# Kernel optimization log

Hardware: AMD Instinct MI355X
Metric: run time of the kernel (lower is better)

## Reference

```python
import jax, jax.numpy as jnp
import numpy as np

B, T, F, D, NL, V = 16, 1024, 80, 512, 3, 28


def _ln(x, g, b, eps=1e-5):
    m = jnp.mean(x, axis=-1, keepdims=True)
    v = jnp.mean((x - m) ** 2, axis=-1, keepdims=True)
    return (x - m) * jax.lax.rsqrt(v + eps) * g + b


def _sru_layer(x, W, wc, bias, g, beta):
    # x: [T, B, din]; W: [din, k*d] (k=4 when din != d, else k=3)
    d = wc.shape[0] // 2
    xn = _ln(x, g, beta)                       # layer_norm=True: LN on layer input
    U = jnp.einsum('tbi,ij->tbj', xn, W)       # [T, B, k*d]
    u0, u1, u2 = U[..., :d], U[..., d:2 * d], U[..., 2 * d:3 * d]
    xres = U[..., 3 * d:4 * d] if W.shape[1] == 4 * d else x  # highway input
    vf, vr = wc[:d], wc[d:]
    bf, br = bias[:d], bias[d:]

    def step(c, inp):
        a0, a1, a2, xr = inp
        f = jax.nn.sigmoid(a1 + vf * c + bf)
        r = jax.nn.sigmoid(a2 + vr * c + br)
        c2 = f * c + (1.0 - f) * a0
        h = r * c2 + (1.0 - r) * xr
        return c2, h

    c0 = jnp.zeros((x.shape[1], d), x.dtype)
    _, h = jax.lax.scan(step, c0, (u0, u1, u2, xres))
    return h


def _lstm_layer(x, wih, whh, bih, bhh):
    # x: [T, B, d]; torch gate order i, f, g, o
    d = whh.shape[1]
    gx = jnp.einsum('tbi,gi->tbg', x, wih) + bih + bhh  # precompute input gates

    def step(carry, gxt):
        h, c = carry
        gts = gxt + h @ whh.T
        i, f, gg, o = jnp.split(gts, 4, axis=-1)
        c2 = jax.nn.sigmoid(f) * c + jax.nn.sigmoid(i) * jnp.tanh(gg)
        h2 = jax.nn.sigmoid(o) * jnp.tanh(c2)
        return (h2, c2), h2

    nb = x.shape[1]
    init = (jnp.zeros((nb, d), x.dtype), jnp.zeros((nb, d), x.dtype))
    _, h = jax.lax.scan(step, init, gx)
    return h


def _forward(x, sru_w0, sru_wc0, sru_b0, sru_ln0_g, sru_ln0_b,
             sru_w, sru_wc, sru_b, sru_ln_g, sru_ln_b,
             lstm_ln_g, lstm_ln_b, lstm_wih, lstm_whh, lstm_bih, lstm_bhh,
             cls_ln_g, cls_ln_b, cls_w):
    h = jnp.transpose(x, (1, 0, 2))  # [T, B, F]
    h = _sru_layer(h, sru_w0, sru_wc0, sru_b0, sru_ln0_g, sru_ln0_b)
    for i in range(sru_w.shape[0]):  # 7 remaining SRU layers (8 total)
        h = _sru_layer(h, sru_w[i], sru_wc[i], sru_b[i], sru_ln_g[i], sru_ln_b[i])
    for i in range(lstm_wih.shape[0]):  # LSTM blocks: LN -> LSTM (dropout off, eval)
        hn = _ln(h, lstm_ln_g[i], lstm_ln_b[i])
        h = _lstm_layer(hn, lstm_wih[i], lstm_whh[i], lstm_bih[i], lstm_bhh[i])
    h = jnp.transpose(h, (1, 0, 2))  # [B, T, D]
    h = _ln(h, cls_ln_g, cls_ln_b)
    return h @ cls_w                 # [B, T, V+1]


def setup_inputs() -> dict:
    key = jax.random.key(0)
    ks = jax.random.split(key, 8)
    n = lambda k, s, sc: jax.random.normal(k, s, jnp.float32) * sc
    sF, sD = 1.0 / np.sqrt(F), 1.0 / np.sqrt(D)
    return {
        'x': n(ks[0], (B, T, F), 1.0),
        'sru_w0': n(ks[1], (F, 4 * D), sF),
        'sru_wc0': n(ks[2], (2 * D,), 0.1),
        'sru_b0': jnp.zeros((2 * D,), jnp.float32),
        'sru_ln0_g': jnp.ones((F,), jnp.float32),
        'sru_ln0_b': jnp.zeros((F,), jnp.float32),
        'sru_w': n(ks[3], (7, D, 3 * D), sD),
        'sru_wc': n(ks[4], (7, 2 * D), 0.1),
        'sru_b': jnp.zeros((7, 2 * D), jnp.float32),
        'sru_ln_g': jnp.ones((7, D), jnp.float32),
        'sru_ln_b': jnp.zeros((7, D), jnp.float32),
        'lstm_ln_g': jnp.ones((NL, D), jnp.float32),
        'lstm_ln_b': jnp.zeros((NL, D), jnp.float32),
        'lstm_wih': n(ks[5], (NL, 4 * D, D), sD),
        'lstm_whh': n(ks[6], (NL, 4 * D, D), sD),
        'lstm_bih': jnp.zeros((NL, 4 * D), jnp.float32),
        'lstm_bhh': jnp.zeros((NL, 4 * D), jnp.float32),
        'cls_ln_g': jnp.ones((D,), jnp.float32),
        'cls_ln_b': jnp.zeros((D,), jnp.float32),
        'cls_w': n(ks[7], (D, V + 1), sD),
    }


def reference(x, sru_w0, sru_wc0, sru_b0, sru_ln0_g, sru_ln0_b,
              sru_w, sru_wc, sru_b, sru_ln_g, sru_ln_b,
              lstm_ln_g, lstm_ln_b, lstm_wih, lstm_whh, lstm_bih, lstm_bhh,
              cls_ln_g, cls_ln_b, cls_w):
    return _forward(x, sru_w0, sru_wc0, sru_b0, sru_ln0_g, sru_ln0_b,
                    sru_w, sru_wc, sru_b, sru_ln_g, sru_ln_b,
                    lstm_ln_g, lstm_ln_b, lstm_wih, lstm_whh, lstm_bih, lstm_bhh,
                    cls_ln_g, cls_ln_b, cls_w)
```

## Files before the change

kernel.cpp:

```cpp
#include <hip/hip_runtime.h>
#include <stdint.h>
#include <stddef.h>

#define B_ 16
#define T_ 1024
#define F_ 80
#define D_ 512
#define M_ 16384
#define VO 29
#define SENT 0x7FC07FC0u

typedef float f32x4 __attribute__((ext_vector_type(4)));
typedef short s16x8 __attribute__((ext_vector_type(8)));
typedef unsigned short u16x8 __attribute__((ext_vector_type(8)));

static __device__ __forceinline__ unsigned short f2bf(float f) {
    union { float f; unsigned u; } v; v.f = f;
    unsigned r = v.u + 0x7FFFu + ((v.u >> 16) & 1u);
    return (unsigned short)(r >> 16);
}
static __device__ __forceinline__ float bf2f(unsigned short h) {
    union { unsigned u; float f; } v; v.u = ((unsigned)h) << 16; return v.f;
}
static __device__ __forceinline__ void split2(float v, unsigned short& hi, unsigned short& lo) {
    hi = f2bf(v);
    lo = f2bf(v - bf2f(hi));
}
static __device__ __forceinline__ float sigm(float x) {
    return 1.0f / (1.0f + __expf(-x));
}
static __device__ __forceinline__ float fast_tanh(float x) {
    return 1.0f - 2.0f / (__expf(2.0f * x) + 1.0f);
}
static __device__ __forceinline__ float wred(float v) {
    #pragma unroll
    for (int off = 1; off < 64; off <<= 1) v += __shfl_xor(v, off, 64);
    return v;
}
static __device__ __forceinline__ float ldf_agent(const float* p) {
    unsigned u = __hip_atomic_load((const unsigned*)p, __ATOMIC_RELAXED, __HIP_MEMORY_SCOPE_AGENT);
    union { unsigned u; float f; } c; c.u = u; return c.f;
}
static __device__ __forceinline__ void stf_agent(float* p, float v) {
    union { float f; unsigned u; } c; c.f = v;
    __hip_atomic_store((unsigned*)p, c.u, __ATOMIC_RELAXED, __HIP_MEMORY_SCOPE_AGENT);
}
static __device__ __forceinline__ void gload16(const void* g, void* lds) {
    __builtin_amdgcn_global_load_lds(
        (const __attribute__((address_space(1))) void*)g,
        (__attribute__((address_space(3))) void*)lds, 16, 0, 0);
}

__global__ __launch_bounds__(256) void conv_w0(const float* __restrict__ W,
        unsigned short* __restrict__ Bh, unsigned short* __restrict__ Bl) {
    int gid = blockIdx.x * 256 + threadIdx.x;
    int n = gid / 96, k = gid - n * 96;
    float v = (k < 80) ? W[(size_t)k * 2048 + n] : 0.0f;
    unsigned short h, l; split2(v, h, l);
    Bh[gid] = h; Bl[gid] = l;
}
__global__ __launch_bounds__(256) void conv_sruw1(const float* __restrict__ W,
        unsigned short* __restrict__ Bh, unsigned short* __restrict__ Bl) {
    int gid = blockIdx.x * 256 + threadIdx.x;
    int n = gid >> 9, k = gid & 511;
    float v = W[(size_t)k * 1536 + n];
    unsigned short h, lo; split2(v, h, lo);
    Bh[gid] = h; Bl[gid] = lo;
}
__global__ __launch_bounds__(256) void conv_split(const float* __restrict__ W,
        unsigned short* __restrict__ Oh, unsigned short* __restrict__ Ol, int n) {
    int gid = blockIdx.x * 256 + threadIdx.x;
    if (gid < n) {
        unsigned short h, l; split2(W[gid], h, l);
        Oh[gid] = h; Ol[gid] = l;
    }
}
__global__ __launch_bounds__(256) void sent_fill(unsigned int* __restrict__ buf, int n) {
    int gid = blockIdx.x * 256 + threadIdx.x;
    if (gid < n)
        __hip_atomic_store(&buf[gid], SENT, __ATOMIC_RELAXED, __HIP_MEMORY_SCOPE_AGENT);
}
__global__ void zero_ctl(unsigned int* c) {
    if (threadIdx.x < 160)
        __hip_atomic_store(&c[threadIdx.x], 0u, __ATOMIC_RELAXED, __HIP_MEMORY_SCOPE_AGENT);
}

__global__ __launch_bounds__(256) void ln80_kernel(const float* __restrict__ x,
        const float* __restrict__ g, const float* __restrict__ bta,
        unsigned short* __restrict__ xh, unsigned short* __restrict__ xl) {
    int w = threadIdx.x >> 6, lane = threadIdx.x & 63;
    int row = blockIdx.x * 4 + w;
    int b = row & 15, t = row >> 4;
    const float* xr = x + ((size_t)b * T_ + t) * F_;
    float v0 = xr[lane];
    float v1 = (lane < 16) ? xr[64 + lane] : 0.0f;
    float mean = wred(v0 + v1) * (1.0f / 80.0f);
    float d0 = v0 - mean;
    float d1 = (lane < 16) ? (v1 - mean) : 0.0f;
    float var = wred(d0 * d0 + d1 * d1) * (1.0f / 80.0f);
    float rstd = rsqrtf(var + 1e-5f);
    float o0 = d0 * rstd * g[lane] + bta[lane];
    unsigned short h, l; split2(o0, h, l);
    xh[(size_t)row * 96 + lane] = h;
    xl[(size_t)row * 96 + lane] = l;
    if (lane < 32) {
        unsigned short hv = 0, lv = 0;
        if (lane < 16) {
            float o1 = d1 * rstd * g[64 + lane] + bta[64 + lane];
            split2(o1, hv, lv);
        }
        xh[(size_t)row * 96 + 64 + lane] = hv;
        xl[(size_t)row * 96 + 64 + lane] = lv;
    }
}

__global__ __launch_bounds__(256) void ln512_bf16(const float* __restrict__ hsrc,
        const float* __restrict__ g, const float* __restrict__ bta,
        unsigned short* __restrict__ oh, unsigned short* __restrict__ ol) {
    int w = threadIdx.x >> 6, lane = threadIdx.x & 63;
    size_t row = (size_t)blockIdx.x * 4 + w;
    const float* hr = hsrc + row * D_;
    float4 p0 = *(const float4*)(hr + lane * 8);
    float4 p1 = *(const float4*)(hr + lane * 8 + 4);
    float s = p0.x + p0.y + p0.z + p0.w + p1.x + p1.y + p1.z + p1.w;
    float mean = wred(s) * (1.0f / 512.0f);
    float d[8] = {p0.x - mean, p0.y - mean, p0.z - mean, p0.w - mean,
                  p1.x - mean, p1.y - mean, p1.z - mean, p1.w - mean};
    float q = 0.f;
    #pragma unroll
    for (int i = 0; i < 8; ++i) q += d[i] * d[i];
    float rstd = rsqrtf(wred(q) * (1.0f / 512.0f) + 1e-5f);
    const float* gp = g + lane * 8;
    const float* bp = bta + lane * 8;
    u16x8 vh, vl;
    #pragma unroll
    for (int i = 0; i < 8; ++i) {
        float o = d[i] * rstd * gp[i] + bp[i];
        unsigned short hh, ll; split2(o, hh, ll);
        vh[i] = hh; vl[i] = ll;
    }
    *(u16x8*)(oh + row * D_ + lane * 8) = vh;
    *(u16x8*)(ol + row * D_ + lane * 8) = vl;
}

__global__ __launch_bounds__(256) void ln512_f32(const float* __restrict__ hsrc,
        const float* __restrict__ g, const float* __restrict__ bta,
        float* __restrict__ o) {
    int w = threadIdx.x >> 6, lane = threadIdx.x & 63;
    size_t row = (size_t)blockIdx.x * 4 + w;
    const float* hr = hsrc + row * D_;
    float4 p0 = *(const float4*)(hr + lane * 8);
    float4 p1 = *(const float4*)(hr + lane * 8 + 4);
    float s = p0.x + p0.y + p0.z + p0.w + p1.x + p1.y + p1.z + p1.w;
    float mean = wred(s) * (1.0f / 512.0f);
    float d[8] = {p0.x - mean, p0.y - mean, p0.z - mean, p0.w - mean,
                  p1.x - mean, p1.y - mean, p1.z - mean, p1.w - mean};
    float q = 0.f;
    #pragma unroll
    for (int i = 0; i < 8; ++i) q += d[i] * d[i];
    float rstd = rsqrtf(wred(q) * (1.0f / 512.0f) + 1e-5f);
    const float* gp = g + lane * 8;
    const float* bp = bta + lane * 8;
    float* op = o + row * D_ + lane * 8;
    #pragma unroll
    for (int i = 0; i < 8; ++i) op[i] = d[i] * rstd * gp[i] + bp[i];
}

__global__ __launch_bounds__(256) void gemm_split(
        const unsigned short* __restrict__ Ah, const unsigned short* __restrict__ Al,
        const unsigned short* __restrict__ Bh, const unsigned short* __restrict__ Bl,
        float* __restrict__ C, int N, int Kp,
        const float* __restrict__ bias0, const float* __restrict__ bias1) {
    __shared__ __align__(16) unsigned short sAh[4096];
    __shared__ __align__(16) unsigned short sAl[4096];
    __shared__ __align__(16) unsigned short sBh[4096];
    __shared__ __align__(16) unsigned short sBl[4096];
    const int tid = threadIdx.x;
    const int wv = tid >> 6, lane = tid & 63;
    const int c_ = lane & 15, r_ = lane >> 4;
    const int wr = wv >> 1, wc = wv & 1;
    const int mBase = blockIdx.y * 128, nBase = blockIdx.x * 128;

    const int row0 = tid >> 2, row1 = 64 + row0;
    const int sp = tid & 3;
    const int x0 = (row0 & 3) ^ ((row0 >> 2) & 3);
    const int x1 = (row1 & 3) ^ ((row1 >> 2) & 3);
    const size_t gA0 = (size_t)(mBase + row0) * Kp + (size_t)((sp ^ x0) * 8);
    const size_t gA1 = (size_t)(mBase + row1) * Kp + (size_t)((sp ^ x1) * 8);
    const size_t gB0 = (size_t)(nBase + row0) * Kp + (size_t)((sp ^ x0) * 8);
    const size_t gB1 = (size_t)(nBase + row1) * Kp + (size_t)((sp ^ x1) * 8);
    const int ldsW = wv * 1024;

    int offA[4], offB[4];
    #pragma unroll
    for (int f = 0; f < 4; ++f) {
        int ra = wr * 64 + f * 16 + c_;
        int xa = (ra & 3) ^ ((ra >> 2) & 3);
        offA[f] = ra * 32 + ((r_ ^ xa) * 8);
        int rb = wc * 64 + f * 16 + c_;
        int xb = (rb & 3) ^ ((rb >> 2) & 3);
        offB[f] = rb * 32 + ((r_ ^ xb) * 8);
    }

    f32x4 acc[4][4] = {};
    for (int kt = 0; kt < Kp; kt += 32) {
        gload16(Ah + gA0 + kt, (char*)sAh + ldsW);
        gload16(Ah + gA1 + kt, (char*)sAh + 4096 + ldsW);
        gload16(Al + gA0 + kt, (char*)sAl + ldsW);
        gload16(Al + gA1 + kt, (char*)sAl + 4096 + ldsW);
        gload16(Bh + gB0 + kt, (char*)sBh + ldsW);
        gload16(Bh + gB1 + kt, (char*)sBh + 4096 + ldsW);
        gload16(Bl + gB0 + kt, (char*)sBl + ldsW);
        gload16(Bl + gB1 + kt, (char*)sBl + 4096 + ldsW);
        __syncthreads();
        s16x8 ah[4], al[4], bh[4], bl[4];
        #pragma unroll
        for (int f = 0; f < 4; ++f) {
            ah[f] = *(const s16x8*)&sAh[offA[f]];
            al[f] = *(const s16x8*)&sAl[offA[f]];
            bh[f] = *(const s16x8*)&sBh[offB[f]];
            bl[f] = *(const s16x8*)&sBl[offB[f]];
        }
        #pragma unroll
        for (int mf = 0; mf < 4; ++mf) {
            #pragma unroll
            for (int nf = 0; nf < 4; ++nf) {
                acc[mf][nf] = __builtin_amdgcn_mfma_f32_16x16x32_bf16(ah[mf], bh[nf], acc[mf][nf], 0, 0, 0);
                acc[mf][nf] = __builtin_amdgcn_mfma_f32_16x16x32_bf16(al[mf], bh[nf], acc[mf][nf], 0, 0, 0);
                acc[mf][nf] = __builtin_amdgcn_mfma_f32_16x16x32_bf16(ah[mf], bl[nf], acc[mf][nf], 0, 0, 0);
            }
        }
        __syncthreads();
    }
    #pragma unroll
    for (int mf = 0; mf < 4; ++mf) {
        #pragma unroll
        for (int r = 0; r < 4; ++r) {
            int m = mBase + wr * 64 + mf * 16 + r_ * 4 + r;
            float* crow = C + (size_t)m * N + nBase + wc * 64;
            #pragma unroll
            for (int nf = 0; nf < 4; ++nf) {
                int n = nBase + wc * 64 + nf * 16 + c_;
                float v = acc[mf][nf][r];
                if (bias0) v += bias0[n];
                if (bias1) v += bias1[n];
                crow[nf * 16 + c_] = v;
            }
        }
    }
}

__global__ __launch_bounds__(64) void sru_rec(const float* __restrict__ U, int NU,
        const float* __restrict__ xprev, const float* __restrict__ wc,
        const float* __restrict__ bias, float* __restrict__ hout) {
    int gid = blockIdx.x * 64 + threadIdx.x;
    int d = gid & (D_ - 1), b = gid >> 9;
    float vf = wc[d], vr = wc[D_ + d];
    float bf = bias[d], br = bias[D_ + d];
    const float* u0 = U + d;
    const float* u1 = U + D_ + d;
    const float* u2 = U + 2 * D_ + d;
    const float* xr;  size_t xstride;
    if (xprev) { xr = xprev + d; xstride = D_; }
    else       { xr = U + 3 * (size_t)D_ + d; xstride = (size_t)NU; }
    float* ho = hout + d;
    float c = 0.f;
    #pragma unroll 4
    for (int t = 0; t < T_; ++t) {
        size_t row = (size_t)(t * 16 + b);
        float a0 = u0[row * NU];
        float a1 = u1[row * NU];
        float a2 = u2[row * NU];
        float xv = xr[row * xstride];
        float f = sigm(a1 + vf * c + bf);
        float r = sigm(a2 + vr * c + br);
        c = f * c + (1.f - f) * a0;
        float h = r * c + (1.f - r) * xv;
        ho[row * D_] = h;
    }
}


template <int MODE>
static __device__ void lstm_role(int wg, const float* gxsrc,
        const unsigned short* Wh, const unsigned short* Wl,
        unsigned* ring, const unsigned* crewflags, unsigned* myLprog,
        const unsigned* consCprog, float* hout) {
    __shared__ __align__(16) unsigned short hH[16][520];
    __shared__ __align__(16) unsigned short hL[16][520];
    __shared__ float G[16][132];
    const int tid = threadIdx.x;
    const int w = tid >> 6, lane = tid & 63;
    const int c_ = lane & 15, r_ = lane >> 4;

    s16x8 bh0[16], bh1[16], bl0[16], bl1[16];
    {
        size_t R0 = (size_t)(w * 512 + wg * 32 + c_) * 512;
        size_t R1 = R0 + 16 * 512;
        #pragma unroll
        for (int ks = 0; ks < 16; ++ks) {
            bh0[ks] = *(const s16x8*)(Wh + R0 + ks * 32 + r_ * 8);
            bh1[ks] = *(const s16x8*)(Wh + R1 + ks * 32 + r_ * 8);
            bl0[ks] = *(const s16x8*)(Wl + R0 + ks * 32 + r_ * 8);
            bl1[ks] = *(const s16x8*)(Wl + R1 + ks * 32 + r_ * 8);
        }
    }
    for (int i = tid; i < 16 * 520; i += 256) {
        ((unsigned short*)hH)[i] = 0;
        ((unsigned short*)hL)[i] = 0;
    }
    const int eb = tid >> 4;
    const int ed = (tid * 2) & 31;
    float cc0 = 0.f, cc1 = 0.f;
    const int col0 = w * 512 + wg * 32 + c_;
    const int hidx = (eb * 512 + wg * 32 + ed) >> 1;

    float gxv0[4], gxv1[4];
    if (MODE == 0) {
        #pragma unroll
        for (int r = 0; r < 4; ++r) {
            int bt = r_ * 4 + r;
            gxv0[r] = gxsrc[(size_t)bt * 2048 + col0];
            gxv1[r] = gxsrc[(size_t)bt * 2048 + col0 + 16];
        }
    } else {
        while (true) {
            int f = (int)__hip_atomic_load(&crewflags[lane & 31],
                                           __ATOMIC_RELAXED, __HIP_MEMORY_SCOPE_AGENT);
            if (__all(f >= 1)) break;
            __builtin_amdgcn_s_sleep(1);
        }
        #pragma unroll
        for (int r = 0; r < 4; ++r) {
            int bt = r_ * 4 + r;
            gxv0[r] = ldf_agent(gxsrc + (size_t)bt * 2048 + col0);
            gxv1[r] = ldf_agent(gxsrc + (size_t)bt * 2048 + col0 + 16);
        }
    }
    int pcur = 0, pnxt = 8192, pthr = 16384;
    __syncthreads();

    for (int t = 0; t < T_; ++t) {
        if (MODE == 1 && tid == 0)
            __hip_atomic_store(&myLprog[wg], (unsigned)t, __ATOMIC_RELAXED, __HIP_MEMORY_SCOPE_AGENT);
        if (consCprog) {
            int lim = t - 1;
            while (true) {
                int p = (int)__hip_atomic_load(&consCprog[lane & 31],
                                               __ATOMIC_RELAXED, __HIP_MEMORY_SCOPE_AGENT);
                if (__all(p >= lim)) break;
                __builtin_amdgcn_s_sleep(2);
            }
        }
        __hip_atomic_store(&ring[pnxt + hidx], SENT, __ATOMIC_RELAXED, __HIP_MEMORY_SCOPE_AGENT);
        __hip_atomic_store(&ring[pnxt + 4096 + hidx], SENT, __ATOMIC_RELAXED, __HIP_MEMORY_SCOPE_AGENT);
        f32x4 acc0 = {0.f, 0.f, 0.f, 0.f};
        f32x4 acc1 = {0.f, 0.f, 0.f, 0.f};
        #pragma unroll
        for (int ks = 0; ks < 16; ++ks) {
            s16x8 ah = *(const s16x8*)&hH[c_][ks * 32 + r_ * 8];
            s16x8 al = *(const s16x8*)&hL[c_][ks * 32 + r_ * 8];
            acc0 = __builtin_amdgcn_mfma_f32_16x16x32_bf16(ah, bh0[ks], acc0, 0, 0, 0);
            acc1 = __builtin_amdgcn_mfma_f32_16x16x32_bf16(ah, bh1[ks], acc1, 0, 0, 0);
            acc0 = __builtin_amdgcn_mfma_f32_16x16x32_bf16(al, bh0[ks], acc0, 0, 0, 0);
            acc1 = __builtin_amdgcn_mfma_f32_16x16x32_bf16(al, bh1[ks], acc1, 0, 0, 0);
            acc0 = __builtin_amdgcn_mfma_f32_16x16x32_bf16(ah, bl0[ks], acc0, 0, 0, 0);
            acc1 = __builtin_amdgcn_mfma_f32_16x16x32_bf16(ah, bl1[ks], acc1, 0, 0, 0);
        }
        #pragma unroll
        for (int r = 0; r < 4; ++r) {
            int bt = r_ * 4 + r;
            G[bt][w * 32 + c_]      = acc0[r] + gxv0[r];
            G[bt][w * 32 + 16 + c_] = acc1[r] + gxv1[r];
        }
        __syncthreads();
        float iv0 = G[eb][ed],     fv0 = G[eb][32 + ed], gv0 = G[eb][64 + ed], ov0 = G[eb][96 + ed];
        float iv1 = G[eb][ed + 1], fv1 = G[eb][33 + ed], gv1 = G[eb][65 + ed], ov1 = G[eb][97 + ed];
        cc0 = sigm(fv0) * cc0 + sigm(iv0) * fast_tanh(gv0);
        cc1 = sigm(fv1) * cc1 + sigm(iv1) * fast_tanh(gv1);
        float h0 = sigm(ov0) * fast_tanh(cc0);
        float h1 = sigm(ov1) * fast_tanh(cc1);
        asm volatile("s_waitcnt vmcnt(0)" ::: "memory");
        unsigned short h0h, h0l, h1h, h1l;
        split2(h0, h0h, h0l); split2(h1, h1h, h1l);
        unsigned packH = (unsigned)h0h | ((unsigned)h1h << 16);
        unsigned packL = (unsigned)h0l | ((unsigned)h1l << 16);
        __hip_atomic_store(&ring[pcur + hidx], packH, __ATOMIC_RELAXED, __HIP_MEMORY_SCOPE_AGENT);
        __hip_atomic_store(&ring[pcur + 4096 + hidx], packL, __ATOMIC_RELAXED, __HIP_MEMORY_SCOPE_AGENT);
        if (hout) {
            size_t orow = (size_t)(t * 16 + eb) * D_ + wg * 32 + ed;
            hout[orow] = h0; hout[orow + 1] = h1;
        }
        if (t == T_ - 1) break;
        if (MODE == 0) {
            const float* gxr = gxsrc + (size_t)((t + 1) * 16) * 2048;
            #pragma unroll
            for (int r = 0; r < 4; ++r) {
                int bt = r_ * 4 + r;
                gxv0[r] = gxr[(size_t)bt * 2048 + col0];
                gxv1[r] = gxr[(size_t)bt * 2048 + col0 + 16];
            }
        } else {
            int need = t + 2;
            while (true) {
                int f = (int)__hip_atomic_load(&crewflags[lane & 31],
                                               __ATOMIC_RELAXED, __HIP_MEMORY_SCOPE_AGENT);
                if (__all(f >= need)) break;
                __builtin_amdgcn_s_sleep(1);
            }
            const float* gs = gxsrc + (size_t)((t + 1) & 3) * 32768;
            #pragma unroll
            for (int r = 0; r < 4; ++r) {
                int bt = r_ * 4 + r;
                gxv0[r] = ldf_agent(gs + (size_t)bt * 2048 + col0);
                gxv1[r] = ldf_agent(gs + (size_t)bt * 2048 + col0 + 16);
            }
        }
        unsigned long long vh[8], vl[8];
        unsigned badm = 0xFFFFu;
        while (true) {
            #pragma unroll
            for (int j = 0; j < 8; ++j) {
                int q = pcur + j * 512 + tid * 2;
                if (badm & (1u << j))
                    vh[j] = __hip_atomic_load((const unsigned long long*)&ring[q],
                                              __ATOMIC_RELAXED, __HIP_MEMORY_SCOPE_AGENT);
                if (badm & (1u << (8 + j)))
                    vl[j] = __hip_atomic_load((const unsigned long long*)&ring[q + 4096],
                                              __ATOMIC_RELAXED, __HIP_MEMORY_SCOPE_AGENT);
            }
            unsigned nb = 0u;
            #pragma unroll
            for (int j = 0; j < 8; ++j) {
                unsigned a0 = (unsigned)vh[j], a1 = (unsigned)(vh[j] >> 32);
                unsigned b0 = (unsigned)vl[j], b1 = (unsigned)(vl[j] >> 32);
                if (((a0 >> 16) == 0x7FC0u) || ((a1 >> 16) == 0x7FC0u)) nb |= 1u << j;
                if (((b0 >> 16) == 0x7FC0u) || ((b1 >> 16) == 0x7FC0u)) nb |= 1u << (8 + j);
            }
            badm = nb;
            if (!__any(badm != 0u)) break;
            __builtin_amdgcn_s_sleep(1);
        }
        #pragma unroll
        for (int j = 0; j < 8; ++j) {
            int q = j * 512 + tid * 2;
            int bb = q >> 8, dd = (q & 255) * 2;
            *(unsigned long long*)&hH[bb][dd] = vh[j];
            *(unsigned long long*)&hL[bb][dd] = vl[j];
        }
        __syncthreads();
        int tmp = pcur; pcur = pnxt; pnxt = pthr; pthr = tmp;
    }
}

static __device__ void crew_role(int cid, const unsigned* srcring, float* gxr,
        unsigned* flags, unsigned* cprog, const unsigned* lprog,
        const unsigned short* WihHp, const unsigned short* WihLp,
        const float* g, const float* bta,
        const float* bihp, const float* bhhp) {
    __shared__ __align__(16) unsigned short xnH[16][520];
    __shared__ __align__(16) unsigned short xnL[16][520];
    const int tid = threadIdx.x;
    const int w = tid >> 6, lane = tid & 63;
    const int c_ = lane & 15, r_ = lane >> 4;
    const int col = cid * 64 + w * 16 + c_;
    const int rr = w * 4 + r_;

    s16x8 bfh[16], bfl[16];
    {
        const unsigned short* wrH = WihHp + (size_t)col * 512;
        const unsigned short* wrL = WihLp + (size_t)col * 512;
        #pragma unroll
        for (int ks = 0; ks < 16; ++ks) {
            bfh[ks] = *(const s16x8*)(wrH + ks * 32 + r_ * 8);
            bfl[ks] = *(const s16x8*)(wrL + ks * 32 + r_ * 8);
        }
    }
    const float bias = bihp[col] + bhhp[col];
    float lg[32], lb[32];
    #pragma unroll
    for (int j = 0; j < 32; ++j) { lg[j] = g[c_ * 32 + j]; lb[j] = bta[c_ * 32 + j]; }

    for (int t = 0; t < T_; ++t) {
        const unsigned* sb = srcring + (t % 3) * 8192;
        const int qi = rr * 256 + c_ * 16;
        unsigned long long vh[8], vl[8];
        unsigned badm = 0xFFFFu;
        while (true) {
            #pragma unroll
            for (int j = 0; j < 8; ++j) {
                if (badm & (1u << j))
                    vh[j] = __hip_atomic_load((const unsigned long long*)&sb[qi + j * 2],
                                              __ATOMIC_RELAXED, __HIP_MEMORY_SCOPE_AGENT);
                if (badm & (1u << (8 + j)))
                    vl[j] = __hip_atomic_load((const unsigned long long*)&sb[4096 + qi + j * 2],
                                              __ATOMIC_RELAXED, __HIP_MEMORY_SCOPE_AGENT);
            }
            unsigned nb = 0u;
            #pragma unroll
            for (int j = 0; j < 8; ++j) {
                unsigned a0 = (unsigned)vh[j], a1 = (unsigned)(vh[j] >> 32);
                unsigned b0 = (unsigned)vl[j], b1 = (unsigned)(vl[j] >> 32);
                if (((a0 >> 16) == 0x7FC0u) || ((a1 >> 16) == 0x7FC0u)) nb |= 1u << j;
                if (((b0 >> 16) == 0x7FC0u) || ((b1 >> 16) == 0x7FC0u)) nb |= 1u << (8 + j);
            }
            badm = nb;
            if (!__any(badm != 0u)) break;
            __builtin_amdgcn_s_sleep(1);
        }
        float x[32];
        #pragma unroll
        for (int k = 0; k < 8; ++k) {
            unsigned ah = (unsigned)vh[k], bh = (unsigned)(vh[k] >> 32);
            unsigned al = (unsigned)vl[k], bl = (unsigned)(vl[k] >> 32);
            x[4 * k + 0] = bf2f((unsigned short)ah) + bf2f((unsigned short)al);
            x[4 * k + 1] = bf2f((unsigned short)(ah >> 16)) + bf2f((unsigned short)(al >> 16));
            x[4 * k + 2] = bf2f((unsigned short)bh) + bf2f((unsigned short)bl);
            x[4 * k + 3] = bf2f((unsigned short)(bh >> 16)) + bf2f((unsigned short)(bl >> 16));
        }
        float s = 0.f;
        #pragma unroll
        for (int j = 0; j < 32; ++j) s += x[j];
        #pragma unroll
        for (int m = 1; m < 16; m <<= 1) s += __shfl_xor(s, m, 64);
        float mean = s * (1.0f / 512.0f);
        float q = 0.f;
        #pragma unroll
        for (int j = 0; j < 32; ++j) { float d = x[j] - mean; q += d * d; }
        #pragma unroll
        for (int m = 1; m < 16; m <<= 1) q += __shfl_xor(q, m, 64);
        float rstd = rsqrtf(q * (1.0f / 512.0f) + 1e-5f);
        u16x8 ph[4], pl[4];
        #pragma unroll
        for (int j = 0; j < 32; ++j) {
            float o = (x[j] - mean) * rstd * lg[j] + lb[j];
            unsigned short hh, ll; split2(o, hh, ll);
            ph[j >> 3][j & 7] = (unsigned short)hh;
            pl[j >> 3][j & 7] = (unsigned short)ll;
        }
        #pragma unroll
        for (int jj = 0; jj < 4; ++jj) {
            *(u16x8*)&xnH[rr][c_ * 32 + jj * 8] = ph[jj];
            *(u16x8*)&xnL[rr][c_ * 32 + jj * 8] = pl[jj];
        }
        __syncthreads();
        if (tid == 0)
            __hip_atomic_store(&cprog[cid], (unsigned)(t + 1), __ATOMIC_RELAXED, __HIP_MEMORY_SCOPE_AGENT);
        f32x4 acc = {bias, bias, bias, bias};
        #pragma unroll
        for (int ks = 0; ks < 16; ++ks) {
            s16x8 axh = *(const s16x8*)&xnH[c_][ks * 32 + r_ * 8];
            s16x8 axl = *(const s16x8*)&xnL[c_][ks * 32 + r_ * 8];
            acc = __builtin_amdgcn_mfma_f32_16x16x32_bf16(axh, bfh[ks], acc, 0, 0, 0);
            acc = __builtin_amdgcn_mfma_f32_16x16x32_bf16(axl, bfh[ks], acc, 0, 0, 0);
            acc = __builtin_amdgcn_mfma_f32_16x16x32_bf16(axh, bfl[ks], acc, 0, 0, 0);
        }
        {
            int lim = t - 3;
            while (true) {
                int p = (int)__hip_atomic_load(&lprog[lane & 15],
                                               __ATOMIC_RELAXED, __HIP_MEMORY_SCOPE_AGENT);
                if (__all(p >= lim)) break;
                __builtin_amdgcn_s_sleep(2);
            }
        }
        float* gs = gxr + (size_t)(t & 3) * 32768;
        #pragma unroll
        for (int r = 0; r < 4; ++r)
            stf_agent(gs + (size_t)(r_ * 4 + r) * 2048 + col, acc[r]);
        asm volatile("s_waitcnt vmcnt(0)" ::: "memory");
        __syncthreads();
        if (tid == 0)
            __hip_atomic_store(&flags[cid], (unsigned)(t + 1), __ATOMIC_RELAXED, __HIP_MEMORY_SCOPE_AGENT);
    }
}

__global__ __launch_bounds__(256, 1) void lstm_pipe(
        const float* __restrict__ gx0,
        const unsigned short* __restrict__ WhhH, const unsigned short* __restrict__ WhhL,
        const unsigned short* __restrict__ WihH, const unsigned short* __restrict__ WihL,
        const float* __restrict__ lng, const float* __restrict__ lnb,
        const float* __restrict__ bih, const float* __restrict__ bhh,
        float* __restrict__ hout,
        unsigned* __restrict__ rings,
        float* __restrict__ gxr,
        unsigned* __restrict__ ctl) {
    const int bid = blockIdx.x;
    const size_t WSL = (size_t)2048 * 512;
    if (bid < 16) {
        lstm_role<0>(bid, gx0, WhhH, WhhL, rings,
                     nullptr, nullptr, ctl + 96, nullptr);
    } else if (bid < 32) {
        lstm_role<1>(bid - 16, gxr, WhhH + WSL, WhhL + WSL, rings + 24576,
                     ctl + 0, ctl + 64, ctl + 128, nullptr);
    } else if (bid < 48) {
        lstm_role<1>(bid - 32, gxr + 4 * 32768, WhhH + 2 * WSL, WhhL + 2 * WSL, rings + 2 * 24576,
                     ctl + 32, ctl + 80, nullptr, hout);
    } else if (bid < 80) {
        crew_role(bid - 48, rings, gxr, ctl + 0, ctl + 96, ctl + 64,
                  WihH, WihL, lng + 512, lnb + 512, bih + 2048, bhh + 2048);
    } else {
        crew_role(bid - 80, rings + 24576, gxr + 4 * 32768, ctl + 32, ctl + 128, ctl + 80,
                  WihH + WSL, WihL + WSL, lng + 1024, lnb + 1024, bih + 4096, bhh + 4096);
    }
}

__global__ __launch_bounds__(256) void cls_gemm(const float* __restrict__ xn,
        const float* __restrict__ wcls, float* __restrict__ out) {
    __shared__ float wl[512][32];
    int tid = threadIdx.x;
    for (int idx = tid; idx < 512 * VO; idx += 256) {
        int k = idx / VO, v = idx - k * VO;
        wl[k][v] = wcls[idx];
    }
    __syncthreads();
    int r8 = tid >> 5, v = tid & 31;
    int row = blockIdx.x * 8 + r8;
    if (v >= VO) return;
    const float* xr = xn + (size_t)row * D_;
    float acc = 0.f;
    #pragma unroll 8
    for (int k = 0; k < 512; ++k) acc += xr[k] * wl[k][v];
    int b = row & 15, t = row >> 4;
    out[((size_t)b * T_ + t) * VO + v] = acc;
}

extern "C" void kernel_launch(void* const* d_in, const int* in_sizes, int n_in,
                              void* d_out, int out_size, void* d_ws, size_t ws_size,
                              hipStream_t stream) {
    const float* x        = (const float*)d_in[0];
    const float* sru_w0   = (const float*)d_in[1];
    const float* sru_wc0  = (const float*)d_in[2];
    const float* sru_b0   = (const float*)d_in[3];
    const float* sru_ln0g = (const float*)d_in[4];
    const float* sru_ln0b = (const float*)d_in[5];
    const float* sru_w    = (const float*)d_in[6];
    const float* sru_wc   = (const float*)d_in[7];
    const float* sru_b    = (const float*)d_in[8];
    const float* sru_lng  = (const float*)d_in[9];
    const float* sru_lnb  = (const float*)d_in[10];
    const float* lstm_lng = (const float*)d_in[11];
    const float* lstm_lnb = (const float*)d_in[12];
    const float* lstm_wih = (const float*)d_in[13];
    const float* lstm_whh = (const float*)d_in[14];
    const float* lstm_bih = (const float*)d_in[15];
    const float* lstm_bhh = (const float*)d_in[16];
    const float* cls_lng  = (const float*)d_in[17];
    const float* cls_lnb  = (const float*)d_in[18];
    const float* cls_w    = (const float*)d_in[19];
    float* out = (float*)d_out;

    char* ws = (char*)d_ws;
    size_t off = 0;
    auto alloc = [&](size_t bytes) -> void* {
        off = (off + 255) & ~(size_t)255;
        void* p = ws + off;
        off += bytes;
        return p;
    };
    float* U             = (float*)alloc((size_t)M_ * 1536 * 4);
    float* hP            = (float*)alloc((size_t)M_ * D_ * 4);
    float* hQ            = (float*)alloc((size_t)M_ * D_ * 4);
    unsigned short* xnh  = (unsigned short*)alloc((size_t)M_ * D_ * 2);
    unsigned short* xnl  = (unsigned short*)alloc((size_t)M_ * D_ * 2);
    unsigned short* w0h  = (unsigned short*)alloc((size_t)2048 * 96 * 2);
    unsigned short* w0l  = (unsigned short*)alloc((size_t)2048 * 96 * 2);
    unsigned short* swh  = (unsigned short*)alloc((size_t)1536 * 512 * 2);
    unsigned short* swl  = (unsigned short*)alloc((size_t)1536 * 512 * 2);
    unsigned short* wihh = (unsigned short*)alloc((size_t)2048 * 512 * 2);
    unsigned short* wihl = (unsigned short*)alloc((size_t)2048 * 512 * 2);
    unsigned short* whh3h = (unsigned short*)alloc((size_t)3 * 2048 * 512 * 2);
    unsigned short* whh3l = (unsigned short*)alloc((size_t)3 * 2048 * 512 * 2);
    unsigned short* wih2h = (unsigned short*)alloc((size_t)2 * 2048 * 512 * 2);
    unsigned short* wih2l = (unsigned short*)alloc((size_t)2 * 2048 * 512 * 2);
    unsigned* rings = (unsigned*)swh;
    float*    gxr   = (float*)swl;
    unsigned* ctl   = (unsigned*)(((char*)swh) + 3 * 24576 * 4);
    float* gx = U;

    hipLaunchKernelGGL(conv_w0, dim3(768), dim3(256), 0, stream, sru_w0, w0h, w0l);

    hipLaunchKernelGGL(ln80_kernel, dim3(4096), dim3(256), 0, stream, x, sru_ln0g, sru_ln0b, xnh, xnl);
    hipLaunchKernelGGL(gemm_split, dim3(2048 / 128, M_ / 128), dim3(256), 0, stream,
                       xnh, xnl, w0h, w0l, gx, 2048, 96, (const float*)nullptr, (const float*)nullptr);
    hipLaunchKernelGGL(sru_rec, dim3(128), dim3(64), 0, stream,
                       gx, 2048, (const float*)nullptr, sru_wc0, sru_b0, hQ);

    float* hcur = hQ; float* hnxt = hP;
    for (int l = 0; l < 7; ++l) {
        hipLaunchKernelGGL(conv_sruw1, dim3(3072), dim3(256), 0, stream,
                           sru_w + (size_t)l * 512 * 1536, swh, swl);
        hipLaunchKernelGGL(ln512_bf16, dim3(4096), dim3(256), 0, stream,
                           hcur, sru_lng + (size_t)l * 512, sru_lnb + (size_t)l * 512, xnh, xnl);
        hipLaunchKernelGGL(gemm_split, dim3(1536 / 128, M_ / 128), dim3(256), 0, stream,
                           xnh, xnl, swh, swl, U, 1536, 512,
                           (const float*)nullptr, (const float*)nullptr);
        hipLaunchKernelGGL(sru_rec, dim3(128), dim3(64), 0, stream,
                           U, 1536, hcur, sru_wc + (size_t)l * 1024, sru_b + (size_t)l * 1024, hnxt);
        float* tmp = hcur; hcur = hnxt; hnxt = tmp;
    }

    hipLaunchKernelGGL(conv_split, dim3(12288), dim3(256), 0, stream,
                       lstm_whh, whh3h, whh3l, 3 * 2048 * 512);
    hipLaunchKernelGGL(conv_split, dim3(8192), dim3(256), 0, stream,
                       lstm_wih + (size_t)2048 * 512, wih2h, wih2l, 2 * 2048 * 512);
    hipLaunchKernelGGL(conv_split, dim3(4096), dim3(256), 0, stream,
                       lstm_wih, wihh, wihl, 2048 * 512);
    hipLaunchKernelGGL(ln512_bf16, dim3(4096), dim3(256), 0, stream,
                       hcur, lstm_lng, lstm_lnb, xnh, xnl);
    hipLaunchKernelGGL(gemm_split, dim3(2048 / 128, M_ / 128), dim3(256), 0, stream,
                       xnh, xnl, wihh, wihl, gx, 2048, 512, lstm_bih, lstm_bhh);
    hipLaunchKernelGGL(sent_fill, dim3(288), dim3(256), 0, stream, rings, 3 * 24576);
    hipLaunchKernelGGL(zero_ctl, dim3(1), dim3(256), 0, stream, ctl);

    hipLaunchKernelGGL(lstm_pipe, dim3(112), dim3(256), 0, stream,
                       gx, whh3h, whh3l, wih2h, wih2l,
                       lstm_lng, lstm_lnb, lstm_bih, lstm_bhh,
                       hQ, rings, gxr, ctl);

    hipLaunchKernelGGL(ln512_f32, dim3(4096), dim3(256), 0, stream, hQ, cls_lng, cls_lnb, (float*)U);
    hipLaunchKernelGGL(cls_gemm, dim3(2048), dim3(256), 0, stream, (const float*)U, cls_w, out);
}
```

Before: 8.930 ms.

## Replace crew-to-LSTM flag handshake with sentinel-tagged gate buffer polling

The crew workgroups no longer publish a per-step progress flag after writing input-gate values. Instead they pre-fill the next slot of a deeper (5-slot) gate ring buffer with a NaN sentinel, and the consuming LSTM workgroups poll the gate values directly until no sentinel remains. This removes one flag round-trip per timestep on the serial LSTM critical path and moves the crew's backpressure wait ahead of its compute. The cost is an extra sentinel-fill launch, more atomic polling traffic, and a reliance on real gate values never matching the sentinel bit pattern.

```diff
diff --git a/kernel.cpp b/kernel.cpp
--- a/kernel.cpp
+++ b/kernel.cpp
@@ -9,6 +9,7 @@
 #define M_ 16384
 #define VO 29
 #define SENT 0x7FC07FC0u
+#define GPH 5
 
 typedef float f32x4 __attribute__((ext_vector_type(4)));
 typedef short s16x8 __attribute__((ext_vector_type(8)));
@@ -36,10 +37,6 @@
     #pragma unroll
     for (int off = 1; off < 64; off <<= 1) v += __shfl_xor(v, off, 64);
     return v;
-}
-static __device__ __forceinline__ float ldf_agent(const float* p) {
-    unsigned u = __hip_atomic_load((const unsigned*)p, __ATOMIC_RELAXED, __HIP_MEMORY_SCOPE_AGENT);
-    union { unsigned u; float f; } c; c.u = u; return c.f;
 }
 static __device__ __forceinline__ void stf_agent(float* p, float v) {
     union { float f; unsigned u; } c; c.f = v;
@@ -284,7 +281,7 @@
 template <int MODE>
 static __device__ void lstm_role(int wg, const float* gxsrc,
         const unsigned short* Wh, const unsigned short* Wl,
-        unsigned* ring, const unsigned* crewflags, unsigned* myLprog,
+        unsigned* ring, unsigned* myLprog,
         const unsigned* consCprog, float* hout) {
     __shared__ __align__(16) unsigned short hH[16][520];
     __shared__ __align__(16) unsigned short hL[16][520];
@@ -324,17 +321,33 @@
             gxv1[r] = gxsrc[(size_t)bt * 2048 + col0 + 16];
         }
     } else {
+        const float* gs = gxsrc;
+        unsigned gv[8];
+        unsigned gb = 0xFFu;
         while (true) {
-            int f = (int)__hip_atomic_load(&crewflags[lane & 31],
-                                           __ATOMIC_RELAXED, __HIP_MEMORY_SCOPE_AGENT);
-            if (__all(f >= 1)) break;
+            #pragma unroll
+            for (int r = 0; r < 4; ++r) {
+                int bt = r_ * 4 + r;
+                if (gb & (1u << r))
+                    gv[r] = __hip_atomic_load((const unsigned*)(gs + (size_t)bt * 2048 + col0),
+                                              __ATOMIC_RELAXED, __HIP_MEMORY_SCOPE_AGENT);
+                if (gb & (1u << (4 + r)))
+                    gv[4 + r] = __hip_atomic_load((const unsigned*)(gs + (size_t)bt * 2048 + col0 + 16),
+                                                  __ATOMIC_RELAXED, __HIP_MEMORY_SCOPE_AGENT);
+            }
+            unsigned nb = 0u;
+            #pragma unroll
+            for (int r = 0; r < 8; ++r)
+                if ((gv[r] >> 16) == 0x7FC0u) nb |= 1u << r;
+            gb = nb;
+            if (!__any(gb != 0u)) break;
             __builtin_amdgcn_s_sleep(1);
         }
         #pragma unroll
         for (int r = 0; r < 4; ++r) {
-            int bt = r_ * 4 + r;
-            gxv0[r] = ldf_agent(gxsrc + (size_t)bt * 2048 + col0);
-            gxv1[r] = ldf_agent(gxsrc + (size_t)bt * 2048 + col0 + 16);
+            union { unsigned u; float f; } c0, c1;
+            c0.u = gv[r]; c1.u = gv[4 + r];
+            gxv0[r] = c0.f; gxv1[r] = c1.f;
         }
     }
     int pcur = 0, pnxt = 8192, pthr = 16384;
@@ -401,19 +414,33 @@
                 gxv1[r] = gxr[(size_t)bt * 2048 + col0 + 16];
             }
         } else {
-            int need = t + 2;
+            const float* gs = gxsrc + (size_t)((t + 1) % GPH) * 32768;
+            unsigned gv[8];
+            unsigned gb = 0xFFu;
             while (true) {
-                int f = (int)__hip_atomic_load(&crewflags[lane & 31],
-                                               __ATOMIC_RELAXED, __HIP_MEMORY_SCOPE_AGENT);
-                if (__all(f >= need)) break;
+                #pragma unroll
+                for (int r = 0; r < 4; ++r) {
+                    int bt = r_ * 4 + r;
+                    if (gb & (1u << r))
+                        gv[r] = __hip_atomic_load((const unsigned*)(gs + (size_t)bt * 2048 + col0),
+                                                  __ATOMIC_RELAXED, __HIP_MEMORY_SCOPE_AGENT);
+                    if (gb & (1u << (4 + r)))
+                        gv[4 + r] = __hip_atomic_load((const unsigned*)(gs + (size_t)bt * 2048 + col0 + 16),
+                                                      __ATOMIC_RELAXED, __HIP_MEMORY_SCOPE_AGENT);
+                }
+                unsigned nb = 0u;
+                #pragma unroll
+                for (int r = 0; r < 8; ++r)
+                    if ((gv[r] >> 16) == 0x7FC0u) nb |= 1u << r;
+                gb = nb;
+                if (!__any(gb != 0u)) break;
                 __builtin_amdgcn_s_sleep(1);
             }
-            const float* gs = gxsrc + (size_t)((t + 1) & 3) * 32768;
             #pragma unroll
             for (int r = 0; r < 4; ++r) {
-                int bt = r_ * 4 + r;
-                gxv0[r] = ldf_agent(gs + (size_t)bt * 2048 + col0);
-                gxv1[r] = ldf_agent(gs + (size_t)bt * 2048 + col0 + 16);
+                union { unsigned u; float f; } c0, c1;
+                c0.u = gv[r]; c1.u = gv[4 + r];
+                gxv0[r] = c0.f; gxv1[r] = c1.f;
             }
         }
         unsigned long long vh[8], vl[8];
@@ -454,7 +481,7 @@
 }
 
 static __device__ void crew_role(int cid, const unsigned* srcring, float* gxr,
-        unsigned* flags, unsigned* cprog, const unsigned* lprog,
+        unsigned* cprog, const unsigned* lprog,
         const unsigned short* WihHp, const unsigned short* WihLp,
         const float* g, const float* bta,
         const float* bihp, const float* bhhp) {
@@ -482,6 +509,22 @@
     for (int j = 0; j < 32; ++j) { lg[j] = g[c_ * 32 + j]; lb[j] = bta[c_ * 32 + j]; }
 
     for (int t = 0; t < T_; ++t) {
+        {
+            int lim = t - 3;
+            while (true) {
+                int p = (int)__hip_atomic_load(&lprog[lane & 15],
+                                               __ATOMIC_RELAXED, __HIP_MEMORY_SCOPE_AGENT);
+                if (__all(p >= lim)) break;
+                __builtin_amdgcn_s_sleep(2);
+            }
+        }
+        {
+            unsigned* rs = (unsigned*)(gxr + (size_t)((t + 1) % GPH) * 32768);
+            #pragma unroll
+            for (int r = 0; r < 4; ++r)
+                __hip_atomic_store(&rs[(size_t)(r_ * 4 + r) * 2048 + col], SENT,
+                                   __ATOMIC_RELAXED, __HIP_MEMORY_SCOPE_AGENT);
+        }
         const unsigned* sb = srcring + (t % 3) * 8192;
         const int qi = rr * 256 + c_ * 16;
         unsigned long long vh[8], vl[8];
@@ -555,23 +598,12 @@
             acc = __builtin_amdgcn_mfma_f32_16x16x32_bf16(axl, bfh[ks], acc, 0, 0, 0);
             acc = __builtin_amdgcn_mfma_f32_16x16x32_bf16(axh, bfl[ks], acc, 0, 0, 0);
         }
-        {
-            int lim = t - 3;
-            while (true) {
-                int p = (int)__hip_atomic_load(&lprog[lane & 15],
-                                               __ATOMIC_RELAXED, __HIP_MEMORY_SCOPE_AGENT);
-                if (__all(p >= lim)) break;
-                __builtin_amdgcn_s_sleep(2);
-            }
-        }
-        float* gs = gxr + (size_t)(t & 3) * 32768;
+        asm volatile("s_waitcnt vmcnt(0)" ::: "memory");
+        float* gs = gxr + (size_t)(t % GPH) * 32768;
         #pragma unroll
         for (int r = 0; r < 4; ++r)
             stf_agent(gs + (size_t)(r_ * 4 + r) * 2048 + col, acc[r]);
-        asm volatile("s_waitcnt vmcnt(0)" ::: "memory");
         __syncthreads();
-        if (tid == 0)
-            __hip_atomic_store(&flags[cid], (unsigned)(t + 1), __ATOMIC_RELAXED, __HIP_MEMORY_SCOPE_AGENT);
     }
 }
 
@@ -587,20 +619,21 @@
         unsigned* __restrict__ ctl) {
     const int bid = blockIdx.x;
     const size_t WSL = (size_t)2048 * 512;
+    const int RNG = 3 * 8192;
     if (bid < 16) {
         lstm_role<0>(bid, gx0, WhhH, WhhL, rings,
-                     nullptr, nullptr, ctl + 96, nullptr);
+                     nullptr, ctl + 96, nullptr);
     } else if (bid < 32) {
-        lstm_role<1>(bid - 16, gxr, WhhH + WSL, WhhL + WSL, rings + 24576,
-                     ctl + 0, ctl + 64, ctl + 128, nullptr);
+        lstm_role<1>(bid - 16, gxr, WhhH + WSL, WhhL + WSL, rings + RNG,
+                     ctl + 64, ctl + 128, nullptr);
     } else if (bid < 48) {
-        lstm_role<1>(bid - 32, gxr + 4 * 32768, WhhH + 2 * WSL, WhhL + 2 * WSL, rings + 2 * 24576,
-                     ctl + 32, ctl + 80, nullptr, hout);
+        lstm_role<1>(bid - 32, gxr + (size_t)GPH * 32768, WhhH + 2 * WSL, WhhL + 2 * WSL,
+                     rings + 2 * RNG, ctl + 80, nullptr, hout);
     } else if (bid < 80) {
-        crew_role(bid - 48, rings, gxr, ctl + 0, ctl + 96, ctl + 64,
+        crew_role(bid - 48, rings, gxr, ctl + 96, ctl + 64,
                   WihH, WihL, lng + 512, lnb + 512, bih + 2048, bhh + 2048);
     } else {
-        crew_role(bid - 80, rings + 24576, gxr + 4 * 32768, ctl + 32, ctl + 128, ctl + 80,
+        crew_role(bid - 80, rings + RNG, gxr + (size_t)GPH * 32768, ctl + 128, ctl + 80,
                   WihH + WSL, WihL + WSL, lng + 1024, lnb + 1024, bih + 4096, bhh + 4096);
     }
 }
@@ -675,7 +708,7 @@
     unsigned short* wih2l = (unsigned short*)alloc((size_t)2 * 2048 * 512 * 2);
     unsigned* rings = (unsigned*)swh;
     float*    gxr   = (float*)swl;
-    unsigned* ctl   = (unsigned*)(((char*)swh) + 3 * 24576 * 4);
+    unsigned* ctl   = (unsigned*)(((char*)swh) + 3 * 3 * 8192 * 4);
     float* gx = U;
 
     hipLaunchKernelGGL(conv_w0, dim3(768), dim3(256), 0, stream, sru_w0, w0h, w0l);
@@ -710,7 +743,8 @@
                        hcur, lstm_lng, lstm_lnb, xnh, xnl);
     hipLaunchKernelGGL(gemm_split, dim3(2048 / 128, M_ / 128), dim3(256), 0, stream,
                        xnh, xnl, wihh, wihl, gx, 2048, 512, lstm_bih, lstm_bhh);
-    hipLaunchKernelGGL(sent_fill, dim3(288), dim3(256), 0, stream, rings, 3 * 24576);
+    hipLaunchKernelGGL(sent_fill, dim3(288), dim3(256), 0, stream, rings, 3 * 3 * 8192);
+    hipLaunchKernelGGL(sent_fill, dim3(1280), dim3(256), 0, stream, (unsigned*)gxr, 2 * GPH * 32768);
     hipLaunchKernelGGL(zero_ctl, dim3(1), dim3(256), 0, stream, ctl);
 
     hipLaunchKernelGGL(lstm_pipe, dim3(112), dim3(256), 0, stream,
```

Result: faster. 8.735 ms (-2.2%).
